# Optimization experiments

Hardware: AMD Instinct MI355X
Metric: run time of the kernel (lower is better)

The kernel has to match this reference:

```python
import jax, jax.numpy as jnp
import numpy as np

B, D, M = 512, 1024, 32768
K, MULTI_K, AUX_K = 32, 128, 64
DEAD_THRESH = 256
MATRYOSHKA_SIZES = [4096, 16384, 32768]


def setup_inputs() -> dict:
    key = jax.random.key(0)
    k0, k1, k2, k3, k4, k5 = jax.random.split(key, 6)
    return {
        "x": jax.random.normal(k0, (B, D), dtype=jnp.float32),
        "W_enc": jax.random.normal(k1, (M, D), dtype=jnp.float32) * 0.02,
        "W_dec": jax.random.normal(k2, (D, M), dtype=jnp.float32) * 0.02,
        "input_bias": jax.random.normal(k3, (D,), dtype=jnp.float32) * 0.01,
        "neuron_bias": jax.random.normal(k4, (M,), dtype=jnp.float32) * 0.01,
        "steps_since_activation": jax.random.randint(k5, (M,), 0, 512, dtype=jnp.int64),
    }


def reference(x, W_enc, W_dec, input_bias, neuron_bias, steps_since_activation):
    xc = x - input_bias                                   # [B, D]
    pre_act = xc @ W_enc.T + neuron_bias                  # [B, M]

    topk_values, topk_indices = jax.lax.top_k(pre_act, K)
    topk_values = jax.nn.relu(topk_values)
    multik_values, multik_indices = jax.lax.top_k(pre_act, MULTI_K)
    multik_values = jax.nn.relu(multik_values)

    rows = jnp.arange(pre_act.shape[0])[:, None]
    activations = jnp.zeros_like(pre_act).at[rows, topk_indices].set(topk_values)
    multik_activations = jnp.zeros_like(pre_act).at[rows, multik_indices].set(multik_values)

    reconstruction = activations @ W_dec.T + input_bias
    multik_reconstruction = multik_activations @ W_dec.T + input_bias

    # matryoshka partial reconstructions (all sizes except the last/full one)
    neuron_ids = jnp.arange(M)
    matryoshka_recons = []
    for m_i in MATRYOSHKA_SIZES[:-1]:
        partial_acts = activations * (neuron_ids < m_i).astype(activations.dtype)
        matryoshka_recons.append(partial_acts @ W_dec.T + input_bias)

    # aux-k over dead neurons (steps incremented by 1 before the mask in torch)
    dead_mask = ((steps_since_activation + 1) > DEAD_THRESH).astype(pre_act.dtype)
    aux_values, aux_indices = jax.lax.top_k(pre_act * dead_mask, AUX_K)
    aux_values = jax.nn.relu(aux_values)

    return (reconstruction, multik_reconstruction,
            matryoshka_recons[0], matryoshka_recons[1],
            topk_indices, topk_values, aux_indices, aux_values)
```

## Files before the change

### kernel.cpp

```cpp
#include <hip/hip_runtime.h>
#include <stdint.h>

#define B_ 512
#define D_ 1024
#define M_ 32768

typedef _Float16 half8 __attribute__((ext_vector_type(8)));
typedef _Float16 half4 __attribute__((ext_vector_type(4)));
typedef float f32x4 __attribute__((ext_vector_type(4)));

__device__ __forceinline__ unsigned f2k(float f) {
    unsigned b = __float_as_uint(f);
    return (b & 0x80000000u) ? ~b : (b | 0x80000000u);
}
__device__ __forceinline__ float k2f(unsigned k) {
    unsigned b = (k & 0x80000000u) ? (k & 0x7FFFFFFFu) : ~k;
    return __uint_as_float(b);
}
__device__ __forceinline__ unsigned long long d2k(double d) {
    unsigned long long b = (unsigned long long)__double_as_longlong(d);
    return (b & 0x8000000000000000ull) ? ~b : (b | 0x8000000000000000ull);
}

__device__ __forceinline__ void gld16(const void* g, void* l) {
    __builtin_amdgcn_global_load_lds(
        (__attribute__((address_space(1))) void*)(uintptr_t)g,
        (__attribute__((address_space(3))) void*)(unsigned)(uintptr_t)l,
        16, 0, 0);
}

__global__ __launch_bounds__(256) void split_x_k(
    const float* __restrict__ x, const float* __restrict__ ib,
    _Float16* __restrict__ xh)
{
    int i = blockIdx.x * 256 + threadIdx.x;
    float4 v = ((const float4*)x)[i];
    float4 bb = ((const float4*)ib)[i & 255];
    float a0 = (v.x - bb.x) * 2048.0f;
    float a1 = (v.y - bb.y) * 2048.0f;
    float a2 = (v.z - bb.z) * 2048.0f;
    float a3 = (v.w - bb.w) * 2048.0f;
    half4 hv = {(_Float16)a0, (_Float16)a1, (_Float16)a2, (_Float16)a3};
    ((half4*)xh)[i] = hv;
}

__global__ __launch_bounds__(256, 6) void enc_tr(
    const _Float16* __restrict__ xhf,
    const float* __restrict__ wenc, const float* __restrict__ nb,
    _Float16* __restrict__ preact,
    const float* __restrict__ wdec, float* __restrict__ wdt)
{
    __shared__ alignas(16) char smem[24576];

    const int tid = threadIdx.x;
    const int chunk = blockIdx.x >> 8;
    const int sub = (chunk >> 1) * 256 + (blockIdx.x & 255);

    if (chunk & 1) {
        float (*ttile)[33] = (float(*)[33])smem;
        const int tx = tid & 31, ty = tid >> 5;
        for (int s = 0; s < 16; ++s) {
            int tix = sub * 16 + s;
            int x0 = (tix & 1023) * 32;
            int y0 = (tix >> 10) * 32;
#pragma unroll
            for (int j = 0; j < 32; j += 8)
                ttile[ty + j][tx] = wdec[(size_t)(y0 + ty + j) * M_ + x0 + tx];
            __syncthreads();
#pragma unroll
            for (int j = 0; j < 32; j += 8)
                wdt[(size_t)(x0 + ty + j) * D_ + y0 + tx] = ttile[tx][ty + j];
            __syncthreads();
        }
        return;
    }

    _Float16* lA0 = (_Float16*)smem;
    _Float16* lB0 = (_Float16*)(smem + 16384);

    const int lane = tid & 63;
    const int wv = tid >> 6;
    const int wvr = wv >> 1;
    const int wvc = wv & 1;

    const int bid = sub;
    const int lb = bid >> 3;
    const int j0 = ((bid & 7) * 64 + (lb >> 2)) * 64;
    const int i0 = (lb & 3) * 128;

    const int ln15 = lane & 15;
    const int kq = (lane >> 4) * 8;

    f32x4 acc1[4][2];
#pragma unroll
    for (int r = 0; r < 4; ++r)
#pragma unroll
        for (int c = 0; c < 2; ++c)
            acc1[r][c] = (f32x4){0.f, 0.f, 0.f, 0.f};

    const int o0 = tid * 16;
    const int o1 = o0 + 4096;
    const int rA0 = o0 >> 6, rA1 = o1 >> 6;
    const int cA0s = (o0 & 63) ^ (((rA0 >> 1) & 3) << 4);
    const int cA1s = (o1 & 63) ^ (((rA1 >> 1) & 3) << 4);

    const int rW = tid >> 2;
    const int c8 = (tid & 3) * 8;
    const int c8s = c8 ^ (((rW >> 1) & 3) << 3);

    const int rowA = wvr * 64 + ln15;
    const int rowB = wvc * 32 + ln15;

#define STAGEA(k0, s)                                                                      \
    do {                                                                                   \
        gld16((const char*)(xhf + (size_t)(i0 + rA0) * 1024 + (k0)) + cA0s, (char*)lA0 + (s) * 8192 + o0); \
        gld16((const char*)(xhf + (size_t)(i0 + rA1) * 1024 + (k0)) + cA1s, (char*)lA0 + (s) * 8192 + o1); \
    } while (0)

#define LOADB(k0)                                                                          \
    do {                                                                                   \
        const float* wp = wenc + (size_t)(j0 + rW) * 1024 + (k0) + c8;                     \
        wv0 = *(const float4*)wp;                                                          \
        wv1 = *(const float4*)(wp + 4);                                                    \
    } while (0)

#define CVT1(idx, f) do { bh[idx] = (_Float16)((f) * 2048.0f); } while (0)

#define WRITEB(s)                                                                          \
    do {                                                                                   \
        half8 bh;                                                                          \
        CVT1(0, wv0.x); CVT1(1, wv0.y); CVT1(2, wv0.z); CVT1(3, wv0.w);                    \
        CVT1(4, wv1.x); CVT1(5, wv1.y); CVT1(6, wv1.z); CVT1(7, wv1.w);                    \
        *(half8*)&lB0[(s) * 2048 + rW * 32 + c8s] = bh;                                    \
    } while (0)

    float4 wv0, wv1;
    LOADB(0);
    asm volatile("s_waitcnt vmcnt(0)" ::: "memory");
    WRITEB(0);
    STAGEA(0, 0);
    LOADB(32);
    STAGEA(32, 1);
    asm volatile("s_waitcnt vmcnt(2)" ::: "memory");
    WRITEB(1);
    asm volatile("s_waitcnt lgkmcnt(0)" ::: "memory");
    __builtin_amdgcn_s_barrier();

    int cur = 0;
    for (int k0 = 0; k0 < 1024; k0 += 32) {
        if (k0 + 64 < 1024) LOADB(k0 + 64);

        half8 aH[4], bH[2];
#pragma unroll
        for (int r = 0; r < 4; ++r) {
            const int ra = rowA + r * 16;
            const int ka = kq ^ (((ra >> 1) & 3) << 3);
            aH[r] = *(const half8*)&lA0[cur * 4096 + ra * 32 + ka];
        }
#pragma unroll
        for (int c = 0; c < 2; ++c) {
            const int rb = rowB + c * 16;
            const int kb = kq ^ (((rb >> 1) & 3) << 3);
            bH[c] = *(const half8*)&lB0[cur * 2048 + rb * 32 + kb];
        }
#pragma unroll
        for (int r = 0; r < 4; ++r)
#pragma unroll
            for (int c = 0; c < 2; ++c)
                acc1[r][c] = __builtin_amdgcn_mfma_f32_16x16x32_f16(aH[r], bH[c], acc1[r][c], 0, 0, 0);

        if (k0 + 32 < 1024) {
            asm volatile("s_waitcnt lgkmcnt(0)" ::: "memory");
            __builtin_amdgcn_s_barrier();

            if (k0 + 64 < 1024) {
                STAGEA(k0 + 64, cur);
                asm volatile("s_waitcnt vmcnt(2)" ::: "memory");
                WRITEB(cur);
            } else {
                asm volatile("s_waitcnt vmcnt(0)" ::: "memory");
            }
            asm volatile("s_waitcnt lgkmcnt(0)" ::: "memory");
            __builtin_amdgcn_s_barrier();
        }
        cur ^= 1;
    }
#undef STAGEA
#undef LOADB
#undef CVT1
#undef WRITEB

    const float s1 = 0x1p-22f;
#pragma unroll
    for (int c = 0; c < 2; ++c) {
        int n = j0 + wvc * 32 + c * 16 + ln15;
        float nbv = nb[n];
#pragma unroll
        for (int r = 0; r < 4; ++r) {
            int mb = i0 + wvr * 64 + r * 16 + (lane >> 4) * 4;
#pragma unroll
            for (int e = 0; e < 4; ++e)
                preact[(size_t)(mb + e) * M_ + n] = (_Float16)(acc1[r][c][e] * s1 + nbv);
        }
    }
}

__global__ __launch_bounds__(1024, 2) void selresdec(
    const _Float16* __restrict__ preact, const int* __restrict__ steps,
    const float* __restrict__ x, const float* __restrict__ ib,
    const float* __restrict__ wenc, const float* __restrict__ nb,
    const float* __restrict__ wdt,
    float* __restrict__ out_tidx, float* __restrict__ out_tval,
    float* __restrict__ out_aidx, float* __restrict__ out_aval,
    float* __restrict__ o_recon, float* __restrict__ o_multik,
    float* __restrict__ o_mat0, float* __restrict__ o_mat1)
{
    __shared__ unsigned histU[4096];
    __shared__ unsigned histM[4096];
    __shared__ unsigned coarseU[256];
    __shared__ unsigned coarseM[256];
    __shared__ unsigned long long candU[512];
    __shared__ unsigned long long candM[512];
    __shared__ double xcs[1024];
    __shared__ double part[160][4];
    __shared__ unsigned long long kU[64];
    __shared__ unsigned long long kM[128];
    __shared__ float vU[64];
    __shared__ float vM[128];
    __shared__ int sidx[128];
    __shared__ float sval[128];
    __shared__ int auxm[96];
    __shared__ int ridx[32];
    __shared__ float rval[32];
    __shared__ unsigned cntU, cntM, thrU, thrM, cbU, cbM, cumU, cumM;

    const int t = threadIdx.x;
    const int b = blockIdx.x;
    const half8* rowh = (const half8*)(preact + (size_t)b * M_);

    for (int i = t; i < 4096; i += 1024) { histU[i] = 0; histM[i] = 0; }
    if (t < 512) { candU[t] = 0ULL; candM[t] = 0ULL; }
    if (t == 0) { cntU = 0; cntM = 0; }
    xcs[t] = (double)x[(size_t)b * 1024 + t] - (double)ib[t];
    if (t < 64)  { kU[t] = 0ULL; vU[t] = 0.f; }
    if (t < 128) { kM[t] = 0ULL; vM[t] = 0.f; }
    __syncthreads();

    unsigned deadmask = 0;
#pragma unroll
    for (int p = 0; p < 4; ++p) {
        int base = 2 * t + 2048 * p;
        int4 s0 = ((const int4*)steps)[base];
        int4 s1 = ((const int4*)steps)[base + 1];
        unsigned mb = 0;
        if (s0.x + 1 > 256) mb |= 1u;
        if (s0.y + 1 > 256) mb |= 2u;
        if (s0.z + 1 > 256) mb |= 4u;
        if (s0.w + 1 > 256) mb |= 8u;
        if (s1.x + 1 > 256) mb |= 16u;
        if (s1.y + 1 > 256) mb |= 32u;
        if (s1.z + 1 > 256) mb |= 64u;
        if (s1.w + 1 > 256) mb |= 128u;
        deadmask |= mb << (p * 8);
    }

    half8 v[4];
#pragma unroll
    for (int p = 0; p < 4; ++p) {
        v[p] = rowh[t + p * 1024];
#pragma unroll
        for (int e = 0; e < 8; ++e) {
            unsigned key = f2k((float)v[p][e]) >> 20;
            atomicAdd(&histU[key], 1u);
            if ((deadmask >> (p * 8 + e)) & 1u) atomicAdd(&histM[key], 1u);
        }
    }
    __syncthreads();

    if (t < 256) {
        unsigned s = 0;
#pragma unroll
        for (int j = 0; j < 16; ++j) s += histU[t * 16 + j];
        coarseU[t] = s;
    } else if (t < 512) {
        int c = t - 256;
        unsigned s = 0;
#pragma unroll
        for (int j = 0; j < 16; ++j) s += histM[c * 16 + j];
        coarseM[c] = s;
    }
    __syncthreads();

    for (int off = 1; off < 256; off <<= 1) {
        unsigned xv = 0;
        if (t < 256)      xv = coarseU[t] + (t + off < 256 ? coarseU[t + off] : 0u);
        else if (t < 512) { int c = t - 256; xv = coarseM[c] + (c + off < 256 ? coarseM[c + off] : 0u); }
        __syncthreads();
        if (t < 256)      coarseU[t] = xv;
        else if (t < 512) coarseM[t - 256] = xv;
        __syncthreads();
    }

    if (t < 256) {
        unsigned S = coarseU[t];
        unsigned Sn = (t < 255) ? coarseU[t + 1] : 0u;
        if (S >= 128u && (t == 255 || Sn < 128u)) { cbU = (unsigned)t; cumU = Sn; }
    } else if (t < 512) {
        int c = t - 256;
        unsigned S = coarseM[c];
        unsigned Sn = (c < 255) ? coarseM[c + 1] : 0u;
        if (S >= 64u && (c == 255 || Sn < 64u)) { cbM = (unsigned)c; cumM = Sn; }
        if (c == 0 && S < 64u) { cbM = 0u; cumM = Sn; }
    }
    __syncthreads();

    if (t == 0) {
        unsigned cum = cumU;
        int base = (int)cbU * 16, tb = base;
        for (int f = base + 15; f >= base; --f) {
            unsigned h = histU[f];
            if (cum + h >= 128u) { tb = f; break; }
            cum += h;
        }
        thrU = (unsigned)tb;
    }
    if (t == 64) {
        unsigned cum = cumM;
        int base = (int)cbM * 16, tb = base;
        for (int f = base + 15; f >= base; --f) {
            unsigned h = histM[f];
            if (cum + h >= 64u) { tb = f; break; }
            cum += h;
        }
        thrM = (unsigned)(tb > 0 ? tb - 1 : 0);
    }
    __syncthreads();

    const unsigned TU = thrU, TM = thrM;

#pragma unroll
    for (int p = 0; p < 4; ++p) {
#pragma unroll
        for (int e = 0; e < 8; ++e) {
            float val = (float)v[p][e];
            unsigned key = f2k(val);
            int m = (t + p * 1024) * 8 + e;
            if ((key >> 20) >= TU) {
                unsigned pz = atomicAdd(&cntU, 1u);
                if (pz < 512u) candU[pz] = ((unsigned long long)key << 32) | (unsigned)(~m);
            }
            if (((deadmask >> (p * 8 + e)) & 1u) && (key >> 20) >= TM) {
                unsigned pz = atomicAdd(&cntM, 1u);
                if (pz < 512u) candM[pz] = ((unsigned long long)key << 32) | (unsigned)(~m);
            }
        }
    }
    __syncthreads();

    {
        unsigned long long* arr = (t < 512) ? candU : candM;
        const unsigned i = (unsigned)t & 511u;
        for (unsigned kk = 2; kk <= 512; kk <<= 1) {
            for (unsigned j = kk >> 1; j > 0; j >>= 1) {
                unsigned ixj = i ^ j;
                if (ixj > i) {
                    bool desc = ((i & kk) == 0);
                    unsigned long long a = arr[i], c = arr[ixj];
                    if (desc ? (a < c) : (a > c)) { arr[i] = c; arr[ixj] = a; }
                }
                unsigned nj = (j > 1) ? (j >> 1) : ((kk << 1) <= 512u ? kk : 0u);
                if (j >= 64 || nj >= 64) __syncthreads();
                else asm volatile("s_waitcnt lgkmcnt(0)" ::: "memory");
            }
        }
    }
    __syncthreads();

    if (t < 128) {
        unsigned long long c = candU[t];
        unsigned m = ~(unsigned)c;
        float vv = k2f((unsigned)(c >> 32));
        sidx[t] = (int)m;
        sval[t] = vv > 0.f ? vv : 0.f;
    }
    if (t < 96) {
        unsigned long long c = candM[t];
        auxm[t] = c ? (int)(~(unsigned)c) : -1;
    }
    __syncthreads();

    if (t < 640) {
        const int ci = t >> 2, q = t & 3;
        int m = (ci < 64) ? sidx[ci] : auxm[ci - 64];
        if (m >= 0) {
            const float* w = wenc + (size_t)m * 1024 + q * 256;
            const double* xq = xcs + q * 256;
            double a0 = 0.0, a1 = 0.0, a2 = 0.0, a3 = 0.0;
            for (int d = 0; d < 256; d += 4) {
                float4 wv = *(const float4*)(w + d);
                a0 = fma((double)wv.x, xq[d + 0], a0);
                a1 = fma((double)wv.y, xq[d + 1], a1);
                a2 = fma((double)wv.z, xq[d + 2], a2);
                a3 = fma((double)wv.w, xq[d + 3], a3);
            }
            part[ci][q] = ((a0 + a1) + (a2 + a3));
        }
    }
    __syncthreads();

    if (t < 160) {
        int m = (t < 64) ? sidx[t] : auxm[t - 64];
        if (m >= 0) {
            double vd = ((part[t][0] + part[t][1]) + (part[t][2] + part[t][3])) + (double)nb[m];
            unsigned long long key = (d2k(vd) & 0xFFFFFFFFFFFF0000ull)
                                   | (unsigned long long)((~(unsigned)m) & 0xFFFFu);
            float vf = (float)vd;
            if (t < 64) { kU[t] = key; vU[t] = vf; }
            else        { kM[t - 64] = key; vM[t - 64] = vf; }
        }
    }
    __syncthreads();

    for (unsigned kk = 2; kk <= 128; kk <<= 1) {
        for (unsigned j = kk >> 1; j > 0; j >>= 1) {
            unsigned i = (unsigned)t, ixj = i ^ j;
            if (kk <= 64 && i < 64 && ixj > i) {
                bool desc = ((i & kk) == 0);
                unsigned long long a = kU[i], c = kU[ixj];
                if (desc ? (a < c) : (a > c)) {
                    kU[i] = c; kU[ixj] = a;
                    float fa = vU[i]; vU[i] = vU[ixj]; vU[ixj] = fa;
                }
            }
            if (i < 128 && ixj > i) {
                bool desc = ((i & kk) == 0);
                unsigned long long a = kM[i], c = kM[ixj];
                if (desc ? (a < c) : (a > c)) {
                    kM[i] = c; kM[ixj] = a;
                    float fa = vM[i]; vM[i] = vM[ixj]; vM[ixj] = fa;
                }
            }
            __syncthreads();
        }
    }

    if (t < 32) {
        unsigned mm = (~(unsigned)kU[t]) & 0xFFFFu;
        float vv = vU[t];
        float rv = vv > 0.f ? vv : 0.f;
        ridx[t] = (int)mm;
        rval[t] = rv;
        out_tidx[b * 32 + t] = (float)mm;
        out_tval[b * 32 + t] = rv;
    }
    if (t < 64) {
        unsigned mm = (~(unsigned)kM[t]) & 0xFFFFu;
        float vv = vM[t];
        out_aidx[b * 64 + t] = (float)mm;
        out_aval[b * 64 + t] = vv > 0.f ? vv : 0.f;
    }
    __syncthreads();

    {
        const int d = t;
        float bias = ib[d];
        float mul = bias, rec = bias, m0 = bias, m1 = bias;
        for (int k = 0; k < 128; ++k) {
            float vv = sval[k];
            float w = wdt[(size_t)sidx[k] * D_ + d];
            mul += vv * w;
        }
        for (int k = 0; k < 32; ++k) {
            int idx = ridx[k];
            float vv = rval[k];
            float w = wdt[(size_t)idx * D_ + d];
            rec += vv * w;
            if (idx < 16384) {
                m1 += vv * w;
                if (idx < 4096) m0 += vv * w;
            }
        }
        size_t o = (size_t)b * D_ + d;
        o_recon[o]  = rec;
        o_multik[o] = mul;
        o_mat0[o]   = m0;
        o_mat1[o]   = m1;
    }
}

extern "C" void kernel_launch(void* const* d_in, const int* in_sizes, int n_in,
                              void* d_out, int out_size, void* d_ws, size_t ws_size,
                              hipStream_t stream)
{
    const float* x     = (const float*)d_in[0];
    const float* wenc  = (const float*)d_in[1];
    const float* wdec  = (const float*)d_in[2];
    const float* ib    = (const float*)d_in[3];
    const float* nb    = (const float*)d_in[4];
    const int*   steps = (const int*)d_in[5];
    float* out = (float*)d_out;

    char* ws = (char*)d_ws;
    _Float16*  preact  = (_Float16*)ws;
    float*     wdt     = (float*)(ws + 67108864);
    _Float16*  xhf     = (_Float16*)(ws + 201326592);

    float* out_recon  = out;
    float* out_multik = out + 524288;
    float* out_mat0   = out + 1048576;
    float* out_mat1   = out + 1572864;
    float* out_tidx   = out + 2097152;
    float* out_tval   = out + 2097152 + 16384;
    float* out_aidx   = out + 2097152 + 32768;
    float* out_aval   = out + 2097152 + 32768 + 32768;

    split_x_k<<<dim3(512), dim3(256), 0, stream>>>(x, ib, xhf);
    enc_tr<<<dim3(4096), dim3(256), 0, stream>>>(xhf, wenc, nb, preact, wdec, wdt);
    selresdec<<<dim3(512), dim3(1024), 0, stream>>>(
        preact, steps, x, ib, wenc, nb, wdt,
        out_tidx, out_tval, out_aidx, out_aval,
        out_recon, out_multik, out_mat0, out_mat1);
}
```

Measured before the change: 533.6 us.

## Store transposed decoder weights in fp16 and stage preact stores through LDS

```diff
diff --git a/kernel.cpp b/kernel.cpp
--- a/kernel.cpp
+++ b/kernel.cpp
@@ -48,7 +48,7 @@
     const _Float16* __restrict__ xhf,
     const float* __restrict__ wenc, const float* __restrict__ nb,
     _Float16* __restrict__ preact,
-    const float* __restrict__ wdec, float* __restrict__ wdt)
+    const float* __restrict__ wdec, _Float16* __restrict__ wdt)
 {
     __shared__ alignas(16) char smem[24576];
 
@@ -57,19 +57,32 @@
     const int sub = (chunk >> 1) * 256 + (blockIdx.x & 255);
 
     if (chunk & 1) {
-        float (*ttile)[33] = (float(*)[33])smem;
-        const int tx = tid & 31, ty = tid >> 5;
-        for (int s = 0; s < 16; ++s) {
-            int tix = sub * 16 + s;
-            int x0 = (tix & 1023) * 32;
-            int y0 = (tix >> 10) * 32;
-#pragma unroll
-            for (int j = 0; j < 32; j += 8)
-                ttile[ty + j][tx] = wdec[(size_t)(y0 + ty + j) * M_ + x0 + tx];
+        float* tile = (float*)smem;
+        const int r = tid >> 2;
+        const int q4 = (tid & 3) * 16;
+        for (int s = 0; s < 4; ++s) {
+            int tix = sub * 4 + s;
+            int x0 = (tix & 511) * 64;
+            int y0 = (tix >> 9) * 64;
+            const float* src = wdec + (size_t)(y0 + r) * M_ + x0 + q4;
+            float4 v0 = *(const float4*)(src + 0);
+            float4 v1 = *(const float4*)(src + 4);
+            float4 v2 = *(const float4*)(src + 8);
+            float4 v3 = *(const float4*)(src + 12);
+            float* dst = &tile[r * 65 + q4];
+            dst[0] = v0.x;  dst[1] = v0.y;  dst[2] = v0.z;  dst[3] = v0.w;
+            dst[4] = v1.x;  dst[5] = v1.y;  dst[6] = v1.z;  dst[7] = v1.w;
+            dst[8] = v2.x;  dst[9] = v2.y;  dst[10] = v2.z; dst[11] = v2.w;
+            dst[12] = v3.x; dst[13] = v3.y; dst[14] = v3.z; dst[15] = v3.w;
             __syncthreads();
-#pragma unroll
-            for (int j = 0; j < 32; j += 8)
-                wdt[(size_t)(x0 + ty + j) * D_ + y0 + tx] = ttile[tx][ty + j];
+            half8 h0, h1;
+#pragma unroll
+            for (int i = 0; i < 8; ++i) h0[i] = (_Float16)tile[(q4 + i) * 65 + r];
+#pragma unroll
+            for (int i = 0; i < 8; ++i) h1[i] = (_Float16)tile[(q4 + 8 + i) * 65 + r];
+            _Float16* od = wdt + (size_t)(x0 + r) * D_ + y0 + q4;
+            *(half8*)(od + 0) = h0;
+            *(half8*)(od + 8) = h1;
             __syncthreads();
         }
         return;
@@ -190,18 +203,29 @@
 #undef CVT1
 #undef WRITEB
 
+    asm volatile("s_waitcnt lgkmcnt(0)" ::: "memory");
+    __builtin_amdgcn_s_barrier();
+    _Float16* ct = (_Float16*)smem;
     const float s1 = 0x1p-22f;
 #pragma unroll
     for (int c = 0; c < 2; ++c) {
-        int n = j0 + wvc * 32 + c * 16 + ln15;
-        float nbv = nb[n];
+        int n = wvc * 32 + c * 16 + ln15;
+        float nbv = nb[j0 + n];
 #pragma unroll
         for (int r = 0; r < 4; ++r) {
-            int mb = i0 + wvr * 64 + r * 16 + (lane >> 4) * 4;
+            int mb = wvr * 64 + r * 16 + (lane >> 4) * 4;
 #pragma unroll
             for (int e = 0; e < 4; ++e)
-                preact[(size_t)(mb + e) * M_ + n] = (_Float16)(acc1[r][c][e] * s1 + nbv);
-        }
+                ct[(mb + e) * 64 + n] = (_Float16)(acc1[r][c][e] * s1 + nbv);
+        }
+    }
+    __syncthreads();
+#pragma unroll
+    for (int s = 0; s < 4; ++s) {
+        int idx = s * 256 + tid;
+        int row = idx >> 3;
+        int off8 = (idx & 7) * 8;
+        *(half8*)(preact + (size_t)(i0 + row) * M_ + j0 + off8) = *(half8*)&ct[row * 64 + off8];
     }
 }
 
@@ -209,7 +233,7 @@
     const _Float16* __restrict__ preact, const int* __restrict__ steps,
     const float* __restrict__ x, const float* __restrict__ ib,
     const float* __restrict__ wenc, const float* __restrict__ nb,
-    const float* __restrict__ wdt,
+    const _Float16* __restrict__ wdt,
     float* __restrict__ out_tidx, float* __restrict__ out_tval,
     float* __restrict__ out_aidx, float* __restrict__ out_aval,
     float* __restrict__ o_recon, float* __restrict__ o_multik,
@@ -467,13 +491,13 @@
         float mul = bias, rec = bias, m0 = bias, m1 = bias;
         for (int k = 0; k < 128; ++k) {
             float vv = sval[k];
-            float w = wdt[(size_t)sidx[k] * D_ + d];
+            float w = (float)wdt[(size_t)sidx[k] * D_ + d];
             mul += vv * w;
         }
         for (int k = 0; k < 32; ++k) {
             int idx = ridx[k];
             float vv = rval[k];
-            float w = wdt[(size_t)idx * D_ + d];
+            float w = (float)wdt[(size_t)idx * D_ + d];
             rec += vv * w;
             if (idx < 16384) {
                 m1 += vv * w;
@@ -502,7 +526,7 @@
 
     char* ws = (char*)d_ws;
     _Float16*  preact  = (_Float16*)ws;
-    float*     wdt     = (float*)(ws + 67108864);
+    _Float16*  wdt     = (_Float16*)(ws + 67108864);
     _Float16*  xhf     = (_Float16*)(ws + 201326592);
 
     float* out_recon  = out;
```

New measurement: 487.8 us. 1.09x faster.
